# Performance work log

Hardware: AMD Instinct MI355X
Metric: run time of the kernel (lower is better)

The kernel has to match this reference:

```python
import jax, jax.numpy as jnp
import numpy as np

N = 255      # 17 joints * 15 time steps
NNZ = 2550   # ~avg degree 10
B = 512


def setup_inputs() -> dict:
    key = jax.random.key(0)
    ks = jax.random.split(key, 24)
    inp = {}
    inp["H"] = jax.random.normal(ks[0], (B, N, 2), jnp.float32)
    inp["sm_values"] = jax.random.uniform(ks[1], (NNZ,), jnp.float32)
    inp["sp_values"] = jax.random.uniform(ks[2], (NNZ,), jnp.float32)
    dims = [2, 400, 300, 100, 300, 400, 2]
    names = ["enc0", "enc1", "enc2", "dec0", "dec1", "dec2"]
    for i, nm in enumerate(names):
        din, dout = dims[i], dims[i + 1]
        inp["W_" + nm] = jax.random.normal(ks[3 + 2 * i], (din, dout), jnp.float32) * (1.0 / np.sqrt(din))
        inp["b_" + nm] = jnp.zeros((dout,), jnp.float32)
    inp["sm_indices"] = jax.random.randint(ks[20], (NNZ, 2), 0, N, dtype=jnp.int32)
    inp["sp_indices"] = jax.random.randint(ks[21], (NNZ, 2), 0, N, dtype=jnp.int32)
    return inp


def _densify(indices, values):
    # scatter sparse COO Laplacian into a tiny [N, N] dense matrix (255x255)
    return jnp.zeros((N, N), values.dtype).at[indices[:, 0], indices[:, 1]].add(values)


def reference(H, sm_values, sp_values,
              W_enc0, b_enc0, W_enc1, b_enc1, W_enc2, b_enc2,
              W_dec0, b_dec0, W_dec1, b_dec1, W_dec2, b_dec2,
              sm_indices, sp_indices):
    DADsm = _densify(sm_indices, sm_values)
    DADsp = _densify(sp_indices, sp_values)
    x = H  # [B, N, d]
    # encoder: Laplacian smoothing = ReLU(DADsm @ (x W + b)), batched over B
    for W, b in ((W_enc0, b_enc0), (W_enc1, b_enc1), (W_enc2, b_enc2)):
        x = jax.nn.relu(jnp.einsum('ij,bjd->bid', DADsm, x @ W + b))
    # decoder: Laplacian sharpening = ReLU(DADsp @ (x W + b))
    for W, b in ((W_dec0, b_dec0), (W_dec1, b_dec1), (W_dec2, b_dec2)):
        x = jax.nn.relu(jnp.einsum('ij,bjd->bid', DADsp, x @ W + b))
    return x
```

## Files before the change

### kernel.cpp

```cpp
#include <hip/hip_runtime.h>
#include <hip/hip_fp16.h>

typedef __half f16;
typedef _Float16 h8 __attribute__((ext_vector_type(8)));
typedef _Float16 h4 __attribute__((ext_vector_type(4)));
typedef _Float16 h2 __attribute__((ext_vector_type(2)));
typedef float f32x4 __attribute__((ext_vector_type(4)));

#define NN 255
#define BB 512
#define TSS 264

static __device__ __forceinline__ f16 f2h(float x) { return __float2half(x); }

union H8u { h8 v; h2 p[4]; };


__global__ void zero_k(float* p, int n) {
    int i = blockIdx.x * 256 + threadIdx.x;
    if (i < n) p[i] = 0.f;
}

__global__ void scatter_k(const int* __restrict__ idx, const float* __restrict__ vals,
                          float* __restrict__ dad, int nnz) {
    int t = blockIdx.x * 256 + threadIdx.x;
    if (t < nnz) atomicAdd(&dad[idx[2 * t] * 256 + idx[2 * t + 1]], vals[t]);
}

__global__ void rowsum_k(const float* __restrict__ dad, float* __restrict__ r) {
    int i = blockIdx.x * 64 + threadIdx.x;
    if (i < 256) {
        float s = 0.f;
        if (i < NN) for (int k = 0; k < NN; k++) s += dad[i * 256 + k];
        r[i] = s;
    }
}

__global__ void convert_dad(const float* __restrict__ dadf, f16* __restrict__ dadp) {
    int i = blockIdx.x * 256 + threadIdx.x;
    int which = i >> 16, rc = i & 65535;
    int node = rc >> 8, k = rc & 255;
    float v = (node < NN) ? dadf[(size_t)which * NN * 256 + rc] : 0.f;
    dadp[(size_t)which * 65536 + (((k >> 3) * 256 + node) << 3) + (k & 7)] = f2h(v);
}

__global__ void convert_wt(const float* __restrict__ W, f16* __restrict__ Wtp,
                           int K, int N, int KPB) {
    int f = blockIdx.x;
    int tile = f >> 6, fl = f & 63;
    int Kpad = KPB * 8;
    for (int k = threadIdx.x; k < Kpad; k += 256) {
        float v = (f < N && k < K) ? W[(size_t)k * N + f] : 0.f;
        Wtp[((((size_t)tile * KPB + (k >> 3)) * 64 + fl) << 3) + (k & 7)] = f2h(v);
    }
}

__global__ __launch_bounds__(256) void dad2_in(const float* __restrict__ dad,
                                               const float* __restrict__ H,
                                               float* __restrict__ T0f) {
    int gw = (blockIdx.x * 256 + threadIdx.x) >> 6;
    int lane = threadIdx.x & 63;
    if (gw >= BB * 256) return;
    int b = gw >> 8, i = gw & 255;
    if (i == NN) {
        if (lane == 0) { T0f[(size_t)gw * 2] = 0.f; T0f[(size_t)gw * 2 + 1] = 0.f; }
        return;
    }
    const float* dr = dad + (size_t)i * 256;
    const float* yb = H + (size_t)b * NN * 2;
    float a0 = 0.f, a1 = 0.f;
    for (int k = lane; k < NN; k += 64) {
        float d = dr[k];
        a0 += d * yb[2 * k];
        a1 += d * yb[2 * k + 1];
    }
#pragma unroll
    for (int off = 32; off > 0; off >>= 1) {
        a0 += __shfl_down(a0, off);
        a1 += __shfl_down(a1, off);
    }
    if (lane == 0) {
        T0f[(size_t)gw * 2 + 0] = a0;
        T0f[(size_t)gw * 2 + 1] = a1;
    }
}

template <int KPB, int CT, bool R2, bool OUTF32>
__global__ __launch_bounds__(256, 4) void fused_layer(
        const f16* __restrict__ X,
        const f16* __restrict__ Wtp,
        const float* __restrict__ bias,
        const f16* __restrict__ dadp,
        void* __restrict__ Xn_,
        int Nout, int SN, int ntiles, int rev,
        const float* __restrict__ T0p,
        const float* __restrict__ rsmp,
        const float* __restrict__ W0f,
        const float* __restrict__ b0f) {
    __shared__ _Float16 T[64 * TSS];
    __shared__ _Float16 WL[R2 ? 1344 : 4];
    const int id = blockIdx.x;
    int s = id >> 3;
    int bq = s / ntiles;
    const int tile = s - bq * ntiles;
    if (rev) bq = 63 - bq;
    const int b = ((id & 7) << 6) + bq;
    const int n0 = tile * 64;
    const int tid = threadIdx.x;
    const int w = tid >> 6;
    const int ln = tid & 15;
    const int q = (tid >> 4) & 3;

    h2 a0s[4], a1s[4], rvs[4];
    if constexpr (R2) {
        for (int i2 = tid; i2 < 448; i2 += 256) {
            _Float16 va = (_Float16)(i2 < 400 ? W0f[i2] : 0.f);
            _Float16 vb = (_Float16)(i2 < 400 ? W0f[400 + i2] : 0.f);
            _Float16 vc = (_Float16)(i2 < 400 ? b0f[i2] : 0.f);
            WL[i2] = va; WL[448 + i2] = vb; WL[896 + i2] = vc;
        }
#pragma unroll
        for (int t = 0; t < 4; t++) {
            int node = 64 * w + 16 * t + ln;
            const float* tp = T0p + ((size_t)b * 256 + node) * 2;
            _Float16 x0 = (_Float16)tp[0];
            _Float16 x1 = (_Float16)tp[1];
            _Float16 rv = (_Float16)rsmp[node];
            a0s[t] = (h2){x0, x0};
            a1s[t] = (h2){x1, x1};
            rvs[t] = (h2){rv, rv};
        }
        __syncthreads();
    }

    f32x4 acc[4][CT];
#pragma unroll
    for (int t = 0; t < 4; t++)
#pragma unroll
        for (int c = 0; c < CT; c++) acc[t][c] = (f32x4){0.f, 0.f, 0.f, 0.f};

    const f16* xb = R2 ? (const f16*)nullptr : X + (size_t)b * KPB * 2048;
    const f16* wp = Wtp + (size_t)tile * KPB * 512;

    h8 afr[2][4];
    if constexpr (!R2) {
#pragma unroll
        for (int t = 0; t < 4; t++)
            afr[0][t] = *(const h8*)(xb + ((q * 256 + 64 * w + 16 * t + ln) << 3));
    }

#pragma unroll
    for (int kb = 0; kb < KPB; kb += 4) {
        const int cur = (kb >> 2) & 1, nxt = cur ^ 1;
        h8 bf[CT];
#pragma unroll
        for (int c = 0; c < CT; c++)
            bf[c] = *(const h8*)(wp + (((kb + q) * 64 + 16 * c + ln) << 3));
        h8 afc[4];
        if constexpr (R2) {
            H8u wa, wb, bl;
            wa.v = *(const h8*)&WL[(kb + q) * 8];
            wb.v = *(const h8*)&WL[448 + (kb + q) * 8];
            bl.v = *(const h8*)&WL[896 + (kb + q) * 8];
            const h2 z2 = (h2){(_Float16)0.f, (_Float16)0.f};
#pragma unroll
            for (int t = 0; t < 4; t++) {
                H8u r;
#pragma unroll
                for (int j = 0; j < 4; j++)
                    r.p[j] = __builtin_elementwise_max(
                        a0s[t] * wa.p[j] + a1s[t] * wb.p[j] + rvs[t] * bl.p[j], z2);
                afc[t] = r.v;
            }
        } else {
            if (kb + 4 < KPB) {
#pragma unroll
                for (int t = 0; t < 4; t++)
                    afr[nxt][t] = *(const h8*)(xb + (((kb + 4 + q) * 256 + 64 * w + 16 * t + ln) << 3));
            }
#pragma unroll
            for (int t = 0; t < 4; t++) afc[t] = afr[cur][t];
        }
#pragma unroll
        for (int c = 0; c < CT; c++)
#pragma unroll
            for (int t = 0; t < 4; t++)
                acc[t][c] = __builtin_amdgcn_mfma_f32_16x16x32_f16(afc[t], bf[c], acc[t][c], 0, 0, 0);
    }

#pragma unroll
    for (int c = 0; c < CT; c++) {
        int fl = 16 * c + ln;
        int gf = n0 + fl;
        float bv = (gf < Nout) ? bias[gf] : 0.f;
#pragma unroll
        for (int t = 0; t < 4; t++) {
            h4 pk;
#pragma unroll
            for (int rg = 0; rg < 4; rg++) pk[rg] = (_Float16)(acc[t][c][rg] + bv);
            *(h4*)&T[fl * TSS + 64 * w + 16 * t + q * 4] = pk;
        }
    }
    __syncthreads();

    f32x4 acc2[CT][4];
#pragma unroll
    for (int f = 0; f < CT; f++)
#pragma unroll
        for (int t = 0; t < 4; t++) acc2[f][t] = (f32x4){0.f, 0.f, 0.f, 0.f};

    h8 b2[2][4];
#pragma unroll
    for (int t = 0; t < 4; t++)
        b2[0][t] = *(const h8*)(dadp + ((q * 256 + 64 * w + 16 * t + ln) << 3));

#pragma unroll
    for (int kb = 0; kb < 32; kb += 4) {
        const int cur = (kb >> 2) & 1, nxt = cur ^ 1;
        if (kb + 4 < 32) {
#pragma unroll
            for (int t = 0; t < 4; t++)
                b2[nxt][t] = *(const h8*)(dadp + (((kb + 4 + q) * 256 + 64 * w + 16 * t + ln) << 3));
        }
        h8 a2[CT];
#pragma unroll
        for (int f = 0; f < CT; f++)
            a2[f] = *(const h8*)&T[(16 * f + ln) * TSS + (kb + q) * 8];
#pragma unroll
        for (int t = 0; t < 4; t++)
#pragma unroll
            for (int f = 0; f < CT; f++)
                acc2[f][t] = __builtin_amdgcn_mfma_f32_16x16x32_f16(a2[f], b2[cur][t], acc2[f][t], 0, 0, 0);
    }

    if (!OUTF32) {
        f16* xn = (f16*)Xn_ + (size_t)b * (SN >> 3) * 2048;
#pragma unroll
        for (int f = 0; f < CT; f++) {
            int fb = n0 + 16 * f + q * 4;
            if (fb >= SN) continue;
            int fb8 = fb >> 3, off = fb & 7;
#pragma unroll
            for (int t = 0; t < 4; t++) {
                int node = 64 * w + 16 * t + ln;
                h4 pk;
#pragma unroll
                for (int rg = 0; rg < 4; rg++) pk[rg] = (_Float16)fmaxf(acc2[f][t][rg], 0.f);
                *(h4*)(xn + (((size_t)fb8 * 256 + node) << 3) + off) = pk;
            }
        }
    } else {
        if (q == 0) {
            float* op = (float*)Xn_;
#pragma unroll
            for (int t = 0; t < 4; t++) {
                int node = 64 * w + 16 * t + ln;
                if (node < NN) {
                    float2 v;
                    v.x = fmaxf(acc2[0][t][0], 0.f);
                    v.y = fmaxf(acc2[0][t][1], 0.f);
                    *(float2*)(op + ((size_t)b * NN + node) * 2) = v;
                }
            }
        }
    }
}


extern "C" void kernel_launch(void* const* d_in, const int* in_sizes, int n_in,
                              void* d_out, int out_size, void* d_ws, size_t ws_size,
                              hipStream_t stream) {
    const float* H   = (const float*)d_in[0];
    const float* W[6]  = {(const float*)d_in[3], (const float*)d_in[5], (const float*)d_in[7],
                          (const float*)d_in[9], (const float*)d_in[11], (const float*)d_in[13]};
    const float* Bv[6] = {(const float*)d_in[4], (const float*)d_in[6], (const float*)d_in[8],
                          (const float*)d_in[10], (const float*)d_in[12], (const float*)d_in[14]};
    const int* smi = (const int*)d_in[15];
    const int* spi = (const int*)d_in[16];

    char* p = (char*)d_ws;
    f16* bufA = (f16*)p;            p += 109051904;
    f16* bufB = (f16*)p;            p += 83886080;
    float* dadsm = (float*)p;       p += 261120;
    float* dadsp = (float*)p;       p += 261120;
    f16* dadpsm = (f16*)p;          p += 131072;
    f16* dadpsp = (f16*)p;          p += 131072;
    f16* Wt1 = (f16*)p;             p += 266240;
    f16* Wt2 = (f16*)p;             p += 81920;
    f16* Wt3 = (f16*)p;             p += 81920;
    f16* Wt4 = (f16*)p;             p += 286720;
    f16* Wt5 = (f16*)p;             p += 53248;
    float* T0f = (float*)p;         p += 1048576;
    float* rsm = (float*)p;         p += 1024;

    zero_k<<<510, 256, 0, stream>>>(dadsm, 2 * NN * 256);
    scatter_k<<<10, 256, 0, stream>>>(smi, (const float*)d_in[1], dadsm, 2550);
    scatter_k<<<10, 256, 0, stream>>>(spi, (const float*)d_in[2], dadsp, 2550);
    rowsum_k<<<4, 64, 0, stream>>>(dadsm, rsm);
    convert_dad<<<512, 256, 0, stream>>>(dadsm, dadpsm);
    convert_wt<<<320, 256, 0, stream>>>(W[1], Wt1, 400, 300, 52);
    convert_wt<<<128, 256, 0, stream>>>(W[2], Wt2, 300, 100, 40);
    convert_wt<<<320, 256, 0, stream>>>(W[3], Wt3, 100, 300, 16);
    convert_wt<<<448, 256, 0, stream>>>(W[4], Wt4, 300, 400, 40);
    convert_wt<<<64, 256, 0, stream>>>(W[5], Wt5, 400, 2, 52);
    dad2_in<<<(BB * 256 * 64) / 256, 256, 0, stream>>>(dadsm, H, T0f);

    fused_layer<52, 4, true,  false><<<BB * 5, 256, 0, stream>>>(
        nullptr, Wt1, Bv[1], dadpsm, bufB, 300, 320, 5, 0, T0f, rsm, W[0], Bv[0]);
    fused_layer<40, 4, false, false><<<BB * 2, 256, 0, stream>>>(
        bufB, Wt2, Bv[2], dadpsm, bufA, 100, 128, 2, 1, nullptr, nullptr, nullptr, nullptr);
    fused_layer<16, 4, false, false><<<BB * 5, 256, 0, stream>>>(
        bufA, Wt3, Bv[3], dadpsp, bufB, 300, 320, 5, 0, nullptr, nullptr, nullptr, nullptr);
    fused_layer<40, 4, false, false><<<BB * 7, 256, 0, stream>>>(
        bufB, Wt4, Bv[4], dadpsp, bufA, 400, 416, 7, 1, nullptr, nullptr, nullptr, nullptr);
    fused_layer<52, 1, false, true ><<<BB * 1, 256, 0, stream>>>(
        bufA, Wt5, Bv[5], dadpsp, d_out, 2, 2, 1, 0, nullptr, nullptr, nullptr, nullptr);
}
```

Measured before the change: 370.4 us.

## Merge layer kernels into persistent megakernel with per-batch dependency counters

The five per-layer launches are replaced by one persistent kernel of 1024 blocks. Each block walks a flat work list across layers and spin-waits on per-batch atomic counters until the previous layer's tiles for its batch are done. This removes inter-kernel gaps and tail effects and lets layers overlap across batches. Setup kernels are also merged into three launches, and the rowsum and dad2 reductions are vectorised. The risk is deadlock or stalls if blocks aren't co-resident, plus spin-wait overhead and possible visibility issues without explicit fences.

Result: slower. 573.5 us (+54.8%).

```diff
diff --git a/kernel.cpp b/kernel.cpp
--- a/kernel.cpp
+++ b/kernel.cpp
@@ -15,69 +15,88 @@
 
 union H8u { h8 v; h2 p[4]; };
 
-
-__global__ void zero_k(float* p, int n) {
-    int i = blockIdx.x * 256 + threadIdx.x;
-    if (i < n) p[i] = 0.f;
-}
-
-__global__ void scatter_k(const int* __restrict__ idx, const float* __restrict__ vals,
-                          float* __restrict__ dad, int nnz) {
-    int t = blockIdx.x * 256 + threadIdx.x;
-    if (t < nnz) atomicAdd(&dad[idx[2 * t] * 256 + idx[2 * t + 1]], vals[t]);
-}
-
-__global__ void rowsum_k(const float* __restrict__ dad, float* __restrict__ r) {
-    int i = blockIdx.x * 64 + threadIdx.x;
-    if (i < 256) {
-        float s = 0.f;
-        if (i < NN) for (int k = 0; k < NN; k++) s += dad[i * 256 + k];
-        r[i] = s;
-    }
-}
-
-__global__ void convert_dad(const float* __restrict__ dadf, f16* __restrict__ dadp) {
-    int i = blockIdx.x * 256 + threadIdx.x;
-    int which = i >> 16, rc = i & 65535;
-    int node = rc >> 8, k = rc & 255;
-    float v = (node < NN) ? dadf[(size_t)which * NN * 256 + rc] : 0.f;
-    dadp[(size_t)which * 65536 + (((k >> 3) * 256 + node) << 3) + (k & 7)] = f2h(v);
-}
-
-__global__ void convert_wt(const float* __restrict__ W, f16* __restrict__ Wtp,
-                           int K, int N, int KPB) {
-    int f = blockIdx.x;
+__device__ __forceinline__ void conv_wt(const float* __restrict__ W, f16* __restrict__ Wtp,
+                                        int K, int N, int KPB, int f, int tid) {
     int tile = f >> 6, fl = f & 63;
     int Kpad = KPB * 8;
-    for (int k = threadIdx.x; k < Kpad; k += 256) {
+    for (int k = tid; k < Kpad; k += 256) {
         float v = (f < N && k < K) ? W[(size_t)k * N + f] : 0.f;
         Wtp[((((size_t)tile * KPB + (k >> 3)) * 64 + fl) << 3) + (k & 7)] = f2h(v);
     }
 }
 
-__global__ __launch_bounds__(256) void dad2_in(const float* __restrict__ dad,
-                                               const float* __restrict__ H,
-                                               float* __restrict__ T0f) {
-    int gw = (blockIdx.x * 256 + threadIdx.x) >> 6;
-    int lane = threadIdx.x & 63;
+__global__ __launch_bounds__(256) void setup1(
+        float* __restrict__ dadsm, unsigned* __restrict__ cnt,
+        const float* W1, const float* W2, const float* W3, const float* W4, const float* W5,
+        f16* Wt1, f16* Wt2, f16* Wt3, f16* Wt4, f16* Wt5) {
+    int bi = blockIdx.x, tid = threadIdx.x;
+    if (bi < 510) {
+        dadsm[bi * 256 + tid] = 0.f;
+    } else if (bi == 510) {
+        for (int i = tid; i < 2048; i += 256) cnt[i] = 0u;
+    } else {
+        int f = bi - 511;
+        if (f < 320) conv_wt(W1, Wt1, 400, 300, 52, f, tid);
+        else if (f < 448) conv_wt(W2, Wt2, 300, 100, 40, f - 320, tid);
+        else if (f < 768) conv_wt(W3, Wt3, 100, 300, 16, f - 448, tid);
+        else if (f < 1216) conv_wt(W4, Wt4, 300, 400, 40, f - 768, tid);
+        else conv_wt(W5, Wt5, 400, 2, 52, f - 1216, tid);
+    }
+}
+
+__global__ void setup2(const int* __restrict__ smi, const float* __restrict__ smv,
+                       const int* __restrict__ spi, const float* __restrict__ spv,
+                       float* __restrict__ dadsm, float* __restrict__ dadsp) {
+    int t = blockIdx.x * 256 + threadIdx.x;
+    if (blockIdx.x < 10) {
+        if (t < 2550) atomicAdd(&dadsm[smi[2 * t] * 256 + smi[2 * t + 1]], smv[t]);
+    } else {
+        t -= 2560;
+        if (t >= 0 && t < 2550) atomicAdd(&dadsp[spi[2 * t] * 256 + spi[2 * t + 1]], spv[t]);
+    }
+}
+
+__global__ __launch_bounds__(256) void setup3(
+        const float* __restrict__ dadsm, f16* __restrict__ dadpsm,
+        float* __restrict__ rsm, const float* __restrict__ H, float* __restrict__ T0f) {
+    int bi = blockIdx.x, tid = threadIdx.x;
+    if (bi < 512) {
+        int i = bi * 256 + tid;
+        int which = i >> 16, rc = i & 65535;
+        int node = rc >> 8, k = rc & 255;
+        float v = (node < NN) ? dadsm[(size_t)which * NN * 256 + rc] : 0.f;
+        dadpsm[(size_t)which * 65536 + (((k >> 3) * 256 + node) << 3) + (k & 7)] = f2h(v);
+        return;
+    }
+    int lane = tid & 63;
+    if (bi < 576) {
+        int i = (bi - 512) * 4 + (tid >> 6);
+        float s = 0.f;
+        if (i < NN) {
+            f32x4 d = ((const f32x4*)(dadsm + (size_t)i * 256))[lane];
+            s = d.x + d.y + d.z + d.w;
+#pragma unroll
+            for (int off = 1; off < 64; off <<= 1) s += __shfl_xor(s, off);
+        }
+        if (lane == 0) rsm[i] = (i < NN) ? s : 0.f;
+        return;
+    }
+    int gw = (bi - 576) * 4 + (tid >> 6);
     if (gw >= BB * 256) return;
     int b = gw >> 8, i = gw & 255;
-    if (i == NN) {
-        if (lane == 0) { T0f[(size_t)gw * 2] = 0.f; T0f[(size_t)gw * 2 + 1] = 0.f; }
-        return;
-    }
-    const float* dr = dad + (size_t)i * 256;
-    const float* yb = H + (size_t)b * NN * 2;
     float a0 = 0.f, a1 = 0.f;
-    for (int k = lane; k < NN; k += 64) {
-        float d = dr[k];
-        a0 += d * yb[2 * k];
-        a1 += d * yb[2 * k + 1];
-    }
-#pragma unroll
-    for (int off = 32; off > 0; off >>= 1) {
-        a0 += __shfl_down(a0, off);
-        a1 += __shfl_down(a1, off);
+    if (i < NN) {
+        f32x4 d = ((const f32x4*)(dadsm + (size_t)i * 256))[lane];
+        const float2* yb2 = (const float2*)(H + (size_t)b * 510);
+        float2 p0 = yb2[4 * lane], p1 = yb2[4 * lane + 1], p2 = yb2[4 * lane + 2];
+        float2 p3 = (lane < 63) ? yb2[4 * lane + 3] : make_float2(0.f, 0.f);
+        a0 = d.x * p0.x + d.y * p1.x + d.z * p2.x + d.w * p3.x;
+        a1 = d.x * p0.y + d.y * p1.y + d.z * p2.y + d.w * p3.y;
+#pragma unroll
+        for (int off = 1; off < 64; off <<= 1) {
+            a0 += __shfl_xor(a0, off);
+            a1 += __shfl_xor(a1, off);
+        }
     }
     if (lane == 0) {
         T0f[(size_t)gw * 2 + 0] = a0;
@@ -86,27 +105,14 @@
 }
 
 template <int KPB, int CT, bool R2, bool OUTF32>
-__global__ __launch_bounds__(256, 4) void fused_layer(
-        const f16* __restrict__ X,
-        const f16* __restrict__ Wtp,
-        const float* __restrict__ bias,
-        const f16* __restrict__ dadp,
-        void* __restrict__ Xn_,
-        int Nout, int SN, int ntiles, int rev,
-        const float* __restrict__ T0p,
-        const float* __restrict__ rsmp,
-        const float* __restrict__ W0f,
-        const float* __restrict__ b0f) {
-    __shared__ _Float16 T[64 * TSS];
-    __shared__ _Float16 WL[R2 ? 1344 : 4];
-    const int id = blockIdx.x;
-    int s = id >> 3;
-    int bq = s / ntiles;
-    const int tile = s - bq * ntiles;
-    if (rev) bq = 63 - bq;
-    const int b = ((id & 7) << 6) + bq;
+__device__ __forceinline__ void layer_work(
+        int b, int tile, _Float16* T, _Float16* WL,
+        const f16* __restrict__ X, const f16* __restrict__ Wtp,
+        const float* __restrict__ bias, const f16* __restrict__ dadp,
+        void* __restrict__ Xn_, int Nout, int SN,
+        const float* T0p, const float* rsmp, const float* W0f, const float* b0f,
+        int tid) {
     const int n0 = tile * 64;
-    const int tid = threadIdx.x;
     const int w = tid >> 6;
     const int ln = tid & 15;
     const int q = (tid >> 4) & 3;
@@ -114,10 +120,9 @@
     h2 a0s[4], a1s[4], rvs[4];
     if constexpr (R2) {
         for (int i2 = tid; i2 < 448; i2 += 256) {
-            _Float16 va = (_Float16)(i2 < 400 ? W0f[i2] : 0.f);
-            _Float16 vb = (_Float16)(i2 < 400 ? W0f[400 + i2] : 0.f);
-            _Float16 vc = (_Float16)(i2 < 400 ? b0f[i2] : 0.f);
-            WL[i2] = va; WL[448 + i2] = vb; WL[896 + i2] = vc;
+            WL[i2]       = (_Float16)(i2 < 400 ? W0f[i2] : 0.f);
+            WL[448 + i2] = (_Float16)(i2 < 400 ? W0f[400 + i2] : 0.f);
+            WL[896 + i2] = (_Float16)(i2 < 400 ? b0f[i2] : 0.f);
         }
 #pragma unroll
         for (int t = 0; t < 4; t++) {
@@ -263,6 +268,58 @@
                 }
             }
         }
+    }
+}
+
+__global__ __launch_bounds__(256, 4) void mega(
+        const f16* __restrict__ Wt1, const f16* __restrict__ Wt2, const f16* __restrict__ Wt3,
+        const f16* __restrict__ Wt4, const f16* __restrict__ Wt5,
+        const float* __restrict__ B1, const float* __restrict__ B2, const float* __restrict__ B3,
+        const float* __restrict__ B4, const float* __restrict__ B5,
+        const f16* __restrict__ dadpsm, const f16* __restrict__ dadpsp,
+        f16* __restrict__ bufA, f16* __restrict__ bufB, float* __restrict__ out,
+        const float* __restrict__ T0f, const float* __restrict__ rsm,
+        const float* __restrict__ W0, const float* __restrict__ b0,
+        unsigned* __restrict__ cnt) {
+    __shared__ _Float16 T[64 * TSS];
+    __shared__ _Float16 WL[1344];
+    const int x = blockIdx.x & 7;
+    const int g = blockIdx.x >> 3;
+    const int tid = threadIdx.x;
+
+    for (int it = g; it < 1280; it += 128) {
+        int L, bq, tile;
+        if (it < 320)       { L = 1; bq = it / 5;          tile = it - bq * 5; }
+        else if (it < 448)  { L = 2; int s = it - 320;  bq = s >> 1; tile = s & 1; }
+        else if (it < 768)  { L = 3; int s = it - 448;  bq = s / 5;  tile = s - bq * 5; }
+        else if (it < 1216) { L = 4; int s = it - 768;  bq = s / 7;  tile = s - bq * 7; }
+        else                { L = 5; bq = it - 1216;    tile = 0; }
+        const int b = (x << 6) | bq;
+
+        if (L > 1) {
+            if (tid == 0) {
+                unsigned need = (L == 2) ? 5u : (L == 3) ? 2u : (L == 4) ? 5u : 7u;
+                unsigned* c = &cnt[(L - 2) * 512 + b];
+                while (atomicAdd(c, 0u) < need) __builtin_amdgcn_s_sleep(2);
+            }
+            __syncthreads();
+        }
+
+        switch (L) {
+            case 1: layer_work<52, 4, true,  false>(b, tile, T, WL, nullptr, Wt1, B1, dadpsm,
+                        bufB, 300, 320, T0f, rsm, W0, b0, tid); break;
+            case 2: layer_work<40, 4, false, false>(b, tile, T, WL, bufB, Wt2, B2, dadpsm,
+                        bufA, 100, 128, nullptr, nullptr, nullptr, nullptr, tid); break;
+            case 3: layer_work<16, 4, false, false>(b, tile, T, WL, bufA, Wt3, B3, dadpsp,
+                        bufB, 300, 320, nullptr, nullptr, nullptr, nullptr, tid); break;
+            case 4: layer_work<40, 4, false, false>(b, tile, T, WL, bufB, Wt4, B4, dadpsp,
+                        bufA, 400, 416, nullptr, nullptr, nullptr, nullptr, tid); break;
+            default: layer_work<52, 1, false, true >(b, tile, T, WL, bufA, Wt5, B5, dadpsp,
+                        out, 2, 2, nullptr, nullptr, nullptr, nullptr, tid); break;
+        }
+
+        __syncthreads();
+        if (tid == 0 && L < 5) atomicAdd(&cnt[(L - 1) * 512 + b], 1u);
     }
 }
 
@@ -292,27 +349,16 @@
     f16* Wt5 = (f16*)p;             p += 53248;
     float* T0f = (float*)p;         p += 1048576;
     float* rsm = (float*)p;         p += 1024;
-
-    zero_k<<<510, 256, 0, stream>>>(dadsm, 2 * NN * 256);
-    scatter_k<<<10, 256, 0, stream>>>(smi, (const float*)d_in[1], dadsm, 2550);
-    scatter_k<<<10, 256, 0, stream>>>(spi, (const float*)d_in[2], dadsp, 2550);
-    rowsum_k<<<4, 64, 0, stream>>>(dadsm, rsm);
-    convert_dad<<<512, 256, 0, stream>>>(dadsm, dadpsm);
-    convert_wt<<<320, 256, 0, stream>>>(W[1], Wt1, 400, 300, 52);
-    convert_wt<<<128, 256, 0, stream>>>(W[2], Wt2, 300, 100, 40);
-    convert_wt<<<320, 256, 0, stream>>>(W[3], Wt3, 100, 300, 16);
-    convert_wt<<<448, 256, 0, stream>>>(W[4], Wt4, 300, 400, 40);
-    convert_wt<<<64, 256, 0, stream>>>(W[5], Wt5, 400, 2, 52);
-    dad2_in<<<(BB * 256 * 64) / 256, 256, 0, stream>>>(dadsm, H, T0f);
-
-    fused_layer<52, 4, true,  false><<<BB * 5, 256, 0, stream>>>(
-        nullptr, Wt1, Bv[1], dadpsm, bufB, 300, 320, 5, 0, T0f, rsm, W[0], Bv[0]);
-    fused_layer<40, 4, false, false><<<BB * 2, 256, 0, stream>>>(
-        bufB, Wt2, Bv[2], dadpsm, bufA, 100, 128, 2, 1, nullptr, nullptr, nullptr, nullptr);
-    fused_layer<16, 4, false, false><<<BB * 5, 256, 0, stream>>>(
-        bufA, Wt3, Bv[3], dadpsp, bufB, 300, 320, 5, 0, nullptr, nullptr, nullptr, nullptr);
-    fused_layer<40, 4, false, false><<<BB * 7, 256, 0, stream>>>(
-        bufB, Wt4, Bv[4], dadpsp, bufA, 400, 416, 7, 1, nullptr, nullptr, nullptr, nullptr);
-    fused_layer<52, 1, false, true ><<<BB * 1, 256, 0, stream>>>(
-        bufA, Wt5, Bv[5], dadpsp, d_out, 2, 2, 1, 0, nullptr, nullptr, nullptr, nullptr);
-}
+    unsigned* cnt = (unsigned*)p;   p += 8192;
+
+    setup1<<<1791, 256, 0, stream>>>(dadsm, cnt, W[1], W[2], W[3], W[4], W[5],
+                                     Wt1, Wt2, Wt3, Wt4, Wt5);
+    setup2<<<20, 256, 0, stream>>>(smi, (const float*)d_in[1], spi, (const float*)d_in[2],
+                                   dadsm, dadsp);
+    setup3<<<576 + 32768, 256, 0, stream>>>(dadsm, dadpsm, rsm, H, T0f);
+
+    mega<<<1024, 256, 0, stream>>>(Wt1, Wt2, Wt3, Wt4, Wt5,
+                                   Bv[1], Bv[2], Bv[3], Bv[4], Bv[5],
+                                   dadpsm, dadpsp, bufA, bufB, (float*)d_out,
+                                   T0f, rsm, W[0], Bv[0], cnt);
+}
```
